# Kernel tuning notes

Hardware: AMD Instinct MI355X
Metric: run time of the kernel (lower is better)

The kernel has to match this reference:

```python
import jax, jax.numpy as jnp
import numpy as np

B, C, N = 16, 256, 2048
CK = int(C * 0.25)  # key/query channels = 64
CV = C              # value_size = 1 -> value channels = C
BN_EPS = 1e-5


def setup_inputs() -> dict:
    key = jax.random.key(0)
    ks = jax.random.split(key, 7)
    sq = lambda fan_in: 1.0 / np.sqrt(fan_in)
    x = jax.random.normal(ks[0], (B, C, N), dtype=jnp.float32)
    # Conv1d(kernel_size=1, bias=False) weights stored as [out_ch, in_ch]
    Wq = jax.random.uniform(ks[1], (CK, C), jnp.float32, -sq(C), sq(C))
    Wk = jax.random.uniform(ks[2], (CK, C), jnp.float32, -sq(C), sq(C))
    Wv = jax.random.uniform(ks[3], (CV, C), jnp.float32, -sq(C), sq(C))
    Wl = jax.random.uniform(ks[4], (C, C), jnp.float32, -sq(C), sq(C))
    gamma = jnp.ones((C,), jnp.float32)
    beta = jnp.zeros((C,), jnp.float32)
    return {"x": x, "Wq": Wq, "Wk": Wk, "Wv": Wv, "Wl": Wl,
            "gamma": gamma, "beta": beta}


def reference(x, Wq, Wk, Wv, Wl, gamma, beta):
    # x: [B, C, N]
    q = jnp.einsum('oc,bcn->bno', Wq, x)   # [B, N, CK]  (q_conv then permute)
    k = jnp.einsum('oc,bcn->bon', Wk, x)   # [B, CK, N]
    v = jnp.einsum('oc,bcn->bno', Wv, x)   # [B, N, CV]  (v_conv then permute)

    w = jnp.einsum('bnk,bkm->bnm', q, k)   # [B, N, N] raw logits
    # NOTE: column-sum divisor uses RAW logits (RHS evaluated before reassignment
    # in the torch source), not the softmax output.
    col_sum = w.sum(axis=1, keepdims=True)                 # [B, 1, N]
    s = jax.nn.softmax(w, axis=-1) / (1e-9 + col_sum)      # [B, N, N]

    att = jnp.einsum('bnm,bmc->bcn', s, v)  # [B, C, N] (matmul + permute back)
    r = x - att                              # offset (residual of attention)

    # lbr: 1x1 conv -> BatchNorm1d (training-mode batch stats) -> ReLU
    h = jnp.einsum('oc,bcn->bon', Wl, r)     # [B, C, N]
    mean = h.mean(axis=(0, 2), keepdims=True)
    var = ((h - mean) ** 2).mean(axis=(0, 2), keepdims=True)  # biased, as BN
    hn = (h - mean) * jax.lax.rsqrt(var + BN_EPS)
    bn = hn * gamma[None, :, None] + beta[None, :, None]
    out = x + jax.nn.relu(bn)
    return out
```

## Files before the change

### kernel.cpp

```cpp
#include <hip/hip_runtime.h>

#define B_ 16
#define C_ 256
#define N_ 2048
#define CK_ 64

using f32x4  = __attribute__((ext_vector_type(4))) float;
using bf16x8 = __attribute__((ext_vector_type(8))) short;
using short4_t = __attribute__((ext_vector_type(4))) short;
using u32x2  = __attribute__((ext_vector_type(2))) unsigned;

static __device__ __forceinline__ float bf2f(short s){
  unsigned u = ((unsigned)(unsigned short)s) << 16;
  float f; __builtin_memcpy(&f, &u, 4); return f;
}
static __device__ __forceinline__ short f2bf(float f){
  unsigned u; __builtin_memcpy(&u, &f, 4);
  unsigned r = (u + 0x7fffu + ((u >> 16) & 1u)) >> 16;
  return (short)(unsigned short)r;
}

static __device__ __forceinline__ int vf_off(int cp, int ck){
  int q = cp >> 1; int ch = (((cp & 1) << 2) | ck) ^ (q & 7);
  return q*128 + ch*16;
}

__global__ void k_prep(const float* __restrict__ Wq, const float* __restrict__ Wk,
                       const float* __restrict__ Wv, const float* __restrict__ Wl,
                       short* __restrict__ Wb, short* __restrict__ Wlf,
                       const float* __restrict__ x, double* __restrict__ xsum){
  int bid = blockIdx.x;
  if(bid < 1024){
    int b = bid >> 6;
    int c = (bid & 63)*4 + (threadIdx.x>>6);
    int l = threadIdx.x & 63;
    const float* row = x + ((size_t)b*C_ + c)*N_;
    double s = 0.0;
    #pragma unroll
    for(int it = 0; it < 8; ++it){
      f32x4 v = *(const f32x4*)(row + it*256 + l*4);
      s += (double)v[0] + (double)v[1] + (double)v[2] + (double)v[3];
    }
    for(int off = 32; off; off >>= 1) s += __shfl_down(s, off);
    if(l == 0) xsum[b*C_ + c] = s;
  } else {
    int i = (bid - 1024)*256 + threadIdx.x;
    if(i < 384*C_){
      int o = i >> 8;
      float v;
      if(o < 64)       v = Wq[i];
      else if(o < 128) v = Wk[i - 64*C_];
      else             v = Wv[i - 128*C_];
      Wb[i] = f2bf(v);
    }
    if(i < C_*C_){
      int o = i >> 8, c = i & 255;
      int dest = (c>>5)*8192 + (o>>4)*512 + ((((c>>3)&3)*16) + (o&15))*8 + (c&7);
      Wlf[dest] = f2bf(Wl[i]);
    }
  }
}

__global__ void k_prep_g2(const double* __restrict__ xsum, const float* __restrict__ Wq,
                          const float* __restrict__ Wk, double* __restrict__ g){
  int b = blockIdx.x;
  __shared__ double xs[C_];
  __shared__ double t[CK_];
  int tid = threadIdx.x;
  xs[tid] = xsum[b*C_ + tid];
  __syncthreads();
  if(tid < CK_){
    double s = 0.0;
    const float* wr = Wq + (size_t)tid*C_;
    for(int c = 0; c < C_; ++c) s += (double)wr[c]*xs[c];
    t[tid] = s;
  }
  __syncthreads();
  double s = 0.0;
  for(int j = 0; j < CK_; ++j) s += (double)Wk[(size_t)j*C_ + tid]*t[j];
  g[b*C_ + tid] = s;
}

#define XROW 328
__global__ __launch_bounds__(256,2) void k_qkv(const float* __restrict__ x,
        const short* __restrict__ Wb, const double* __restrict__ gg,
        short* __restrict__ qbuf, short* __restrict__ kf, short* __restrict__ vf,
        short* __restrict__ xTb){
  int b = blockIdx.y; int n0 = blockIdx.x*64;
  int tid = threadIdx.x, w = tid>>6, l = tid&63, lo = l&15, g = l>>4;
  __shared__ __attribute__((aligned(16))) short xT[64*XROW];
  __shared__ double gs[C_];
  __shared__ double csum2[256][4];
  __shared__ float inv_lds[64];
  const float* xb = x + (size_t)b*C_*N_;
  gs[tid] = gg[b*C_ + tid];
  __syncthreads();
  int pp2 = tid >> 4, cg = tid & 15;
  double cs[4] = {0.0, 0.0, 0.0, 0.0};
  #pragma unroll
  for(int cc = 0; cc < 8; ++cc){
    int ci = cc*32 + 2*pp2;
    f32x4 x0 = *(const f32x4*)(xb + (size_t)ci*N_ + n0 + 4*cg);
    f32x4 x1 = *(const f32x4*)(xb + (size_t)(ci+1)*N_ + n0 + 4*cg);
    #pragma unroll
    for(int jq = 0; jq < 4; ++jq){
      cs[jq] += (double)x0[jq]*gs[ci] + (double)x1[jq]*gs[ci+1];
      unsigned pr = (unsigned)(unsigned short)f2bf(x0[jq])
                  | (((unsigned)(unsigned short)f2bf(x1[jq]))<<16);
      *(unsigned*)(&xT[(4*cg + jq)*XROW + cc*40 + 2*pp2]) = pr;
    }
  }
  csum2[tid][0] = cs[0]; csum2[tid][1] = cs[1];
  csum2[tid][2] = cs[2]; csum2[tid][3] = cs[3];
  __syncthreads();
  if(tid < 64){
    int cgq = tid >> 2, jq = tid & 3;
    double tot = 0.0;
    #pragma unroll
    for(int k = 0; k < 16; ++k) tot += csum2[k*16 + cgq][jq];
    inv_lds[tid] = (float)(1.0/(1e-9 + tot));
  }

  f32x4 acc[6][4];
  #pragma unroll
  for(int oi=0;oi<6;++oi) for(int nj=0;nj<4;++nj) acc[oi][nj]=(f32x4){0.f,0.f,0.f,0.f};
  int n2 = tid>>2, ii2 = tid&3;
  short* xtb = xTb + ((size_t)b*N_ + n0)*C_;
  #pragma unroll
  for(int cc = 0; cc < 8; ++cc){
    *(bf16x8*)(xtb + (size_t)n2*C_ + cc*32 + 8*ii2) =
        *(const bf16x8*)(&xT[n2*XROW + cc*40 + 8*ii2]);
    bf16x8 bfr[4];
    #pragma unroll
    for(int nj = 0; nj < 4; ++nj)
      bfr[nj] = *(const bf16x8*)(&xT[(nj*16 + lo)*XROW + cc*40 + 8*g]);
    #pragma unroll
    for(int oi = 0; oi < 6; ++oi){
      int o = w*96 + oi*16 + lo;
      bf16x8 af = *(const bf16x8*)(Wb + (size_t)o*C_ + cc*32 + 8*g);
      #pragma unroll
      for(int nj = 0; nj < 4; ++nj)
        acc[oi][nj] = __builtin_amdgcn_mfma_f32_16x16x32_bf16(af, bfr[nj], acc[oi][nj], 0,0,0);
    }
  }
  __syncthreads();

  short* qb  = qbuf + (size_t)b*N_*64;
  short* kfb = kf   + (size_t)b*N_*64;
  short* vfb = vf   + (size_t)b*C_*N_;
  #pragma unroll
  for(int oi = 0; oi < 6; ++oi){
    int obase = w*96 + oi*16;
    for(int nj = 0; nj < 4; ++nj){
      int n = n0 + nj*16 + lo;
      if(obase < 64){
        short4_t pk;
        #pragma unroll
        for(int r = 0; r < 4; ++r) pk[r] = f2bf(acc[oi][nj][r]);
        *(short4_t*)(qb + (size_t)n*64 + obase + 4*g) = pk;
      } else if(obase < 128){
        int C0 = obase - 64 + 4*g;
        int mt = (n0>>4) + nj;
        int h  = C0 >> 5;
        int lanep = ((C0>>3)&3)*16 + lo;
        short4_t pk;
        #pragma unroll
        for(int r = 0; r < 4; ++r) pk[r] = f2bf(acc[oi][nj][r]);
        *(short4_t*)(kfb + ((size_t)(mt*2 + h)*64 + lanep)*8 + (C0&4)) = pk;
      } else {
        float iv = inv_lds[nj*16 + lo];
        int ckk = (n>>3)&3, wi = n&7, mc = n>>5;
        #pragma unroll
        for(int r = 0; r < 4; ++r){
          int cp = obase - 128 + 4*g + r;
          vfb[(size_t)mc*8192 + (vf_off(cp, ckk)>>1) + wi] = f2bf(acc[oi][nj][r]*iv);
        }
      }
    }
  }
}
#undef XROW

__global__ __launch_bounds__(256,2) void k_attn(const short* __restrict__ qbuf,
        const short* __restrict__ kf, const short* __restrict__ vf,
        short* __restrict__ att){
  int d = blockIdx.x;
  int xcd = d & 7, j = d >> 3;
  int b = xcd*2 + (j >> 5);
  int n0 = (j & 31)*64;
  int tid = threadIdx.x;
  int w = tid>>6, l = tid&63, lo = l&15, g = l>>4;

  __shared__ short vlds[2][16384];
  __shared__ short plds[4096];
  __shared__ float rs_lds[64];

  const short* qb  = qbuf + (size_t)b*N_*64;
  const short* kfb = kf   + (size_t)b*N_*64;
  const short* vfb = vf   + (size_t)b*C_*N_;

  bf16x8 qa0, qa1;
  {
    const short* qrow = qb + (size_t)(n0 + w*16 + lo)*64;
    qa0 = *(const bf16x8*)(qrow + 8*g);
    qa1 = *(const bf16x8*)(qrow + 32 + 8*g);
  }
  int paoff[4][2], bvoff[4][2], pw[4];
  #pragma unroll
  for(int rt = 0; rt < 4; ++rt)
    #pragma unroll
    for(int mh = 0; mh < 2; ++mh)
      paoff[rt][mh] = (rt*16 + lo)*128 + (((mh*4 + g) ^ (lo&7))*16);
  #pragma unroll
  for(int jj = 0; jj < 4; ++jj)
    #pragma unroll
    for(int mh = 0; mh < 2; ++mh)
      bvoff[jj][mh] = mh*16384 + vf_off(w*64 + jj*16 + lo, g);
  #pragma unroll
  for(int tt = 0; tt < 4; ++tt)
    pw[tt] = (w*16 + lo)*128 + (((tt*2 + (g>>1)) ^ (lo&7))*16) + (g&1)*8;

  const short* kl   = kfb + l*8;
  const short* vsrc = vfb + w*2048 + l*8;

  f32x4 oacc[4][4];
  #pragma unroll
  for(int rt=0;rt<4;++rt) for(int jj=0;jj<4;++jj) oacc[rt][jj]=(f32x4){0.f,0.f,0.f,0.f};
  float srow = 0.f;

  bf16x8 kA0,kA1,kA2,kA3,kA4,kA5,kA6,kA7;
  bf16x8 kB0,kB1,kB2,kB3,kB4,kB5,kB6,kB7;

#define LOADK(S, MC) { const short* kp = kl + (size_t)((MC)&31)*4096; \
    k##S##0 = *(const bf16x8*)(kp);        k##S##1 = *(const bf16x8*)(kp + 512); \
    k##S##2 = *(const bf16x8*)(kp + 1024); k##S##3 = *(const bf16x8*)(kp + 1536); \
    k##S##4 = *(const bf16x8*)(kp + 2048); k##S##5 = *(const bf16x8*)(kp + 2560); \
    k##S##6 = *(const bf16x8*)(kp + 3072); k##S##7 = *(const bf16x8*)(kp + 3584); }
#define GLLDS(SRC, DST) __builtin_amdgcn_global_load_lds( \
    (const __attribute__((address_space(1))) void*)(SRC), \
    (__attribute__((address_space(3))) void*)(DST), 16, 0, 0)
#define VDMA(MC, NB) { const short* vs = vsrc + (size_t)(2*(MC))*8192; \
    char* dst = (char*)&vlds[NB][0] + w*4096; \
    GLLDS(vs,        dst);        GLLDS(vs +  512, dst + 1024); \
    GLLDS(vs + 1024, dst + 2048); GLLDS(vs + 1536, dst + 3072); \
    GLLDS(vs + 8192,  dst + 16384); GLLDS(vs + 8704,  dst + 17408); \
    GLLDS(vs + 9216,  dst + 18432); GLLDS(vs + 9728,  dst + 19456); }
#define QKT(S, TT, KE, KO) { \
    f32x4 a = (f32x4){0.f,0.f,0.f,0.f}; \
    a = __builtin_amdgcn_mfma_f32_16x16x32_bf16(k##S##KE, qa0, a, 0,0,0); \
    a = __builtin_amdgcn_mfma_f32_16x16x32_bf16(k##S##KO, qa1, a, 0,0,0); \
    float e[4]; \
    _Pragma("unroll") \
    for(int r = 0; r < 4; ++r) e[r] = __builtin_exp2f(fmaf(a[r], 1.44269504f, -17.3123405f)); \
    srow += e[0]+e[1]+e[2]+e[3]; \
    unsigned p0, p1; \
    asm("v_cvt_pk_bf16_f32 %0, %1, %2" : "=v"(p0) : "v"(e[0]), "v"(e[1])); \
    asm("v_cvt_pk_bf16_f32 %0, %1, %2" : "=v"(p1) : "v"(e[2]), "v"(e[3])); \
    { u32x2 pv = {p0, p1}; *(u32x2*)((char*)&plds[0] + pw[TT]) = pv; } }

  LOADK(A, 0);
  LOADK(B, 1);
  VDMA(0, 0);

#define BODY(BUF, S, MC) { \
    VDMA(((MC)+1)&31, (BUF)^1); \
    QKT(S, 0, 0, 1); QKT(S, 1, 2, 3); QKT(S, 2, 4, 5); QKT(S, 3, 6, 7); \
    LOADK(S, (MC)+2); \
    __builtin_amdgcn_sched_barrier(0); \
    asm volatile("s_waitcnt vmcnt(16) lgkmcnt(0)" ::: "memory"); \
    __builtin_amdgcn_s_barrier(); \
    __builtin_amdgcn_sched_barrier(0); \
    __builtin_amdgcn_s_setprio(1); \
    _Pragma("unroll") \
    for(int mh = 0; mh < 2; ++mh){ \
      bf16x8 pa[4], bv[4]; \
      _Pragma("unroll") \
      for(int rt = 0; rt < 4; ++rt) pa[rt] = *(const bf16x8*)((char*)&plds[0] + paoff[rt][mh]); \
      _Pragma("unroll") \
      for(int jj = 0; jj < 4; ++jj) bv[jj] = *(const bf16x8*)((char*)&vlds[BUF][0] + bvoff[jj][mh]); \
      _Pragma("unroll") \
      for(int rt = 0; rt < 4; ++rt) \
        _Pragma("unroll") \
        for(int jj = 0; jj < 4; ++jj) \
          oacc[rt][jj] = __builtin_amdgcn_mfma_f32_16x16x32_bf16(pa[rt], bv[jj], oacc[rt][jj], 0,0,0); \
    } \
    __builtin_amdgcn_s_setprio(0); \
    __builtin_amdgcn_sched_barrier(0); \
    asm volatile("s_waitcnt lgkmcnt(0)" ::: "memory"); \
    __builtin_amdgcn_s_barrier(); \
    __builtin_amdgcn_sched_barrier(0); }

  #pragma unroll 1
  for(int it = 0; it < 16; ++it){
    BODY(0, A, 2*it);
    BODY(1, B, 2*it + 1);
  }
#undef BODY
#undef QKT
#undef VDMA
#undef GLLDS
#undef LOADK

  float S = srow;
  S += __shfl_xor(S, 16);
  S += __shfl_xor(S, 32);
  if(l < 16) rs_lds[w*16 + l] = 1.f/(S + 1e-30f);
  __syncthreads();
  float rinvs[4][4];
  #pragma unroll
  for(int rt = 0; rt < 4; ++rt)
    #pragma unroll
    for(int r = 0; r < 4; ++r) rinvs[rt][r] = rs_lds[rt*16 + 4*g + r];

  short* attb = att + (size_t)b*N_*C_;
  #pragma unroll
  for(int rt = 0; rt < 4; ++rt)
    #pragma unroll
    for(int jj = 0; jj < 4; ++jj)
      #pragma unroll
      for(int r = 0; r < 4; ++r){
        int n = n0 + rt*16 + 4*g + r;
        int c = w*64 + jj*16 + lo;
        attb[(size_t)n*C_ + c] = f2bf(oacc[rt][jj][r]*rinvs[rt][r]);
      }
}

__global__ __launch_bounds__(256,2) void k_hgemm(const short* __restrict__ xTb,
        const short* __restrict__ att, const short* __restrict__ Wlf,
        short* __restrict__ h, float* __restrict__ part){
  int b = blockIdx.y; int n0 = blockIdx.x*64;
  int bid = b*32 + blockIdx.x;
  int tid = threadIdx.x, w = tid>>6, l = tid&63, lo = l&15, g = l>>4;
  __shared__ __attribute__((aligned(16))) short rT[64*C_];
  const short* xtb = xTb + ((size_t)b*N_ + n0)*C_;
  const short* atb = att + ((size_t)b*N_ + n0)*C_;
  int half = l >> 5, ch = l & 31;
  #pragma unroll
  for(int k = 0; k < 8; ++k){
    int n = k*8 + w*2 + half;
    size_t off = (size_t)n*C_ + ch*8;
    bf16x8 xv = *(const bf16x8*)(xtb + off);
    bf16x8 av = *(const bf16x8*)(atb + off);
    bf16x8 rv;
    #pragma unroll
    for(int jq = 0; jq < 8; ++jq) rv[jq] = f2bf(bf2f(xv[jq]) - bf2f(av[jq]));
    *(bf16x8*)(&rT[n*C_ + ((ch ^ (n&7))*8)]) = rv;
  }
  __syncthreads();

  f32x4 acc[4][4];
  #pragma unroll
  for(int ot=0;ot<4;++ot) for(int nj=0;nj<4;++nj) acc[ot][nj]=(f32x4){0.f,0.f,0.f,0.f};
  #pragma unroll
  for(int cb = 0; cb < 8; ++cb){
    bf16x8 bfr[4];
    #pragma unroll
    for(int nj = 0; nj < 4; ++nj)
      bfr[nj] = *(const bf16x8*)(&rT[(nj*16 + lo)*C_ + (((cb*4 + g) ^ (lo&7))*8)]);
    #pragma unroll
    for(int ot = 0; ot < 4; ++ot){
      bf16x8 af = *(const bf16x8*)(Wlf + ((size_t)(cb*16 + w*4 + ot))*512 + l*8);
      #pragma unroll
      for(int nj = 0; nj < 4; ++nj)
        acc[ot][nj] = __builtin_amdgcn_mfma_f32_16x16x32_bf16(af, bfr[nj], acc[ot][nj], 0,0,0);
    }
  }
  short* hb = h + (size_t)b*N_*C_;
  #pragma unroll
  for(int ot = 0; ot < 4; ++ot)
    for(int nj = 0; nj < 4; ++nj){
      int n = n0 + nj*16 + lo;
      short4_t pk;
      #pragma unroll
      for(int r = 0; r < 4; ++r) pk[r] = f2bf(acc[ot][nj][r]);
      *(short4_t*)(&hb[(size_t)n*C_ + w*64 + ot*16 + 4*g]) = pk;
    }
  float* pr_ = part + (size_t)bid*512;
  #pragma unroll
  for(int ot = 0; ot < 4; ++ot){
    float s4[4] = {0,0,0,0}, q4[4] = {0,0,0,0};
    for(int nj = 0; nj < 4; ++nj)
      #pragma unroll
      for(int r = 0; r < 4; ++r){ float v = acc[ot][nj][r]; s4[r] += v; q4[r] += v*v; }
    #pragma unroll
    for(int r = 0; r < 4; ++r){
      float ss = s4[r], qq = q4[r];
      for(int msk = 1; msk < 16; msk <<= 1){ ss += __shfl_xor(ss, msk); qq += __shfl_xor(qq, msk); }
      if(lo == 0){
        int o = w*64 + ot*16 + 4*g + r;
        pr_[o] = ss;
        pr_[256 + o] = qq;
      }
    }
  }
}

__global__ void k_bnfin(const float* __restrict__ part,
                        const float* __restrict__ gamma, const float* __restrict__ beta,
                        float* __restrict__ bnsc, float* __restrict__ bnsh){
  __shared__ float ls[4][512];
  int t = threadIdx.x; int o = t & 255, seg = t >> 8;
  float s = 0.f, q = 0.f;
  for(int r = seg*128; r < seg*128 + 128; ++r){
    s += part[(size_t)r*512 + o];
    q += part[(size_t)r*512 + 256 + o];
  }
  ls[seg][o] = s; ls[seg][256 + o] = q;
  __syncthreads();
  if(t < 256){
    float S = ls[0][t] + ls[1][t] + ls[2][t] + ls[3][t];
    float Q = ls[0][256+t] + ls[1][256+t] + ls[2][256+t] + ls[3][256+t];
    float cnt = (float)(B_*N_);
    float mean = S/cnt;
    float var  = Q/cnt - mean*mean;
    float is   = rsqrtf(var + 1e-5f);
    float sc   = gamma[t]*is;
    bnsc[t] = sc;
    bnsh[t] = beta[t] - mean*sc;
  }
}

__global__ void k_final(const float* __restrict__ x, const short* __restrict__ h,
                        const float* __restrict__ bnsc, const float* __restrict__ bnsh,
                        float* __restrict__ out){
  int b = blockIdx.z, c0 = blockIdx.y*64, n0 = blockIdx.x*64;
  int tid = threadIdx.x;
  __shared__ float ht[64][65];
  {
    int n = tid>>2, ii = tid&3;
    #pragma unroll
    for(int p = 0; p < 2; ++p){
      int coff = 32*p + 8*ii;
      bf16x8 hv = *(const bf16x8*)(h + ((size_t)(b*N_ + n0 + n))*C_ + c0 + coff);
      #pragma unroll
      for(int jq = 0; jq < 8; ++jq) ht[n][coff + jq] = bf2f(hv[jq]);
    }
  }
  __syncthreads();
  int c = tid>>2, i2 = tid&3;
  float sc = bnsc[c0 + c], sh = bnsh[c0 + c];
  const float* xr = x + ((size_t)b*C_ + c0 + c)*N_ + n0 + 16*i2;
  float* orow = out + ((size_t)b*C_ + c0 + c)*N_ + n0 + 16*i2;
  #pragma unroll
  for(int k = 0; k < 16; k += 4){
    f32x4 xv = *(const f32x4*)(xr + k);
    f32x4 ov;
    #pragma unroll
    for(int jq = 0; jq < 4; ++jq){
      float bn = ht[16*i2 + k + jq][c]*sc + sh;
      ov[jq] = xv[jq] + fmaxf(bn, 0.f);
    }
    *(f32x4*)(orow + k) = ov;
  }
}

extern "C" void kernel_launch(void* const* d_in, const int* in_sizes, int n_in,
                              void* d_out, int out_size, void* d_ws, size_t ws_size,
                              hipStream_t stream){
  const float* x     = (const float*)d_in[0];
  const float* Wq    = (const float*)d_in[1];
  const float* Wk    = (const float*)d_in[2];
  const float* Wv    = (const float*)d_in[3];
  const float* Wl    = (const float*)d_in[4];
  const float* gamma = (const float*)d_in[5];
  const float* beta  = (const float*)d_in[6];
  float* out = (float*)d_out;

  char* p = (char*)d_ws;
  double* g    = (double*)p; p += (size_t)B_*C_*8;
  double* xsum = (double*)p; p += (size_t)B_*C_*8;
  short* Wb   = (short*)p;  p += (size_t)384*C_*2;
  short* Wlf  = (short*)p;  p += (size_t)C_*C_*2;
  short* qbuf = (short*)p;  p += (size_t)B_*N_*64*2;
  short* kf   = (short*)p;  p += (size_t)B_*N_*64*2;
  short* vf   = (short*)p;  p += (size_t)B_*C_*N_*2;
  short* xTb  = (short*)p;  p += (size_t)B_*N_*C_*2;
  short* att  = (short*)p;  p += (size_t)B_*N_*C_*2;
  float* part = (float*)p;  p += (size_t)512*512*4;
  float* bnsc = (float*)p;  p += C_*4;
  float* bnsh = (float*)p;  p += C_*4;
  short* h = vf;

  k_prep   <<<1408, 256, 0, stream>>>(Wq, Wk, Wv, Wl, Wb, Wlf, x, xsum);
  k_prep_g2<<<B_, 256, 0, stream>>>(xsum, Wq, Wk, g);
  k_qkv    <<<dim3(N_/64, B_), 256, 0, stream>>>(x, Wb, g, qbuf, kf, vf, xTb);
  k_attn   <<<512, 256, 0, stream>>>(qbuf, kf, vf, att);
  k_hgemm  <<<dim3(N_/64, B_), 256, 0, stream>>>(xTb, att, Wlf, h, part);
  k_bnfin  <<<1, 1024, 0, stream>>>(part, gamma, beta, bnsc, bnsh);
  k_final  <<<dim3(N_/64, C_/64, B_), 256, 0, stream>>>(x, h, bnsc, bnsh, out);
}
```

Baseline: 143.8 us.

## Store h channel-major from hgemm via LDS transpose, simplify final kernel

The hgemm kernel now writes h in [B,C,N] layout, transposing accumulators through the reused LDS tile with a swizzle and storing 16-byte coalesced rows. The final BN/ReLU/residual kernel then becomes a simple row-wise streaming kernel with no LDS transpose or sync. This moves the transpose cost into hgemm, adding two barriers and LDS traffic there, in exchange for cheaper, fully coalesced epilogue loads and stores.

```diff
diff --git a/kernel.cpp b/kernel.cpp
--- a/kernel.cpp
+++ b/kernel.cpp
@@ -327,7 +327,7 @@
 
 __global__ __launch_bounds__(256,2) void k_hgemm(const short* __restrict__ xTb,
         const short* __restrict__ att, const short* __restrict__ Wlf,
-        short* __restrict__ h, float* __restrict__ part){
+        short* __restrict__ hT, float* __restrict__ part){
   int b = blockIdx.y; int n0 = blockIdx.x*64;
   int bid = b*32 + blockIdx.x;
   int tid = threadIdx.x, w = tid>>6, l = tid&63, lo = l&15, g = l>>4;
@@ -365,16 +365,6 @@
         acc[ot][nj] = __builtin_amdgcn_mfma_f32_16x16x32_bf16(af, bfr[nj], acc[ot][nj], 0,0,0);
     }
   }
-  short* hb = h + (size_t)b*N_*C_;
-  #pragma unroll
-  for(int ot = 0; ot < 4; ++ot)
-    for(int nj = 0; nj < 4; ++nj){
-      int n = n0 + nj*16 + lo;
-      short4_t pk;
-      #pragma unroll
-      for(int r = 0; r < 4; ++r) pk[r] = f2bf(acc[ot][nj][r]);
-      *(short4_t*)(&hb[(size_t)n*C_ + w*64 + ot*16 + 4*g]) = pk;
-    }
   float* pr_ = part + (size_t)bid*512;
   #pragma unroll
   for(int ot = 0; ot < 4; ++ot){
@@ -391,6 +381,28 @@
         pr_[o] = ss;
         pr_[256 + o] = qq;
       }
+    }
+  }
+  __syncthreads();
+  #pragma unroll
+  for(int ot = 0; ot < 4; ++ot)
+    #pragma unroll
+    for(int nj = 0; nj < 4; ++nj)
+      #pragma unroll
+      for(int r = 0; r < 4; ++r){
+        int o = w*64 + ot*16 + 4*g + r;
+        int n = nj*16 + lo;
+        rT[o*64 + (n ^ (((o>>2)&3)*16))] = f2bf(acc[ot][nj][r]);
+      }
+  __syncthreads();
+  short* hTb = hT + (size_t)b*C_*N_ + n0;
+  {
+    int ro = tid >> 3, li = tid & 7;
+    #pragma unroll
+    for(int pss = 0; pss < 8; ++pss){
+      int o = pss*32 + ro;
+      bf16x8 v = *(const bf16x8*)(&rT[o*64 + ((li*8) ^ (((o>>2)&3)*16))]);
+      *(bf16x8*)(hTb + (size_t)o*N_ + li*8) = v;
     }
   }
 }
@@ -420,38 +432,27 @@
   }
 }
 
-__global__ void k_final(const float* __restrict__ x, const short* __restrict__ h,
+__global__ void k_final(const float* __restrict__ x, const short* __restrict__ hT,
                         const float* __restrict__ bnsc, const float* __restrict__ bnsh,
                         float* __restrict__ out){
-  int b = blockIdx.z, c0 = blockIdx.y*64, n0 = blockIdx.x*64;
-  int tid = threadIdx.x;
-  __shared__ float ht[64][65];
-  {
-    int n = tid>>2, ii = tid&3;
-    #pragma unroll
-    for(int p = 0; p < 2; ++p){
-      int coff = 32*p + 8*ii;
-      bf16x8 hv = *(const bf16x8*)(h + ((size_t)(b*N_ + n0 + n))*C_ + c0 + coff);
-      #pragma unroll
-      for(int jq = 0; jq < 8; ++jq) ht[n][coff + jq] = bf2f(hv[jq]);
-    }
-  }
-  __syncthreads();
-  int c = tid>>2, i2 = tid&3;
-  float sc = bnsc[c0 + c], sh = bnsh[c0 + c];
-  const float* xr = x + ((size_t)b*C_ + c0 + c)*N_ + n0 + 16*i2;
-  float* orow = out + ((size_t)b*C_ + c0 + c)*N_ + n0 + 16*i2;
-  #pragma unroll
-  for(int k = 0; k < 16; k += 4){
-    f32x4 xv = *(const f32x4*)(xr + k);
-    f32x4 ov;
-    #pragma unroll
-    for(int jq = 0; jq < 4; ++jq){
-      float bn = ht[16*i2 + k + jq][c]*sc + sh;
-      ov[jq] = xv[jq] + fmaxf(bn, 0.f);
-    }
-    *(f32x4*)(orow + k) = ov;
-  }
+  int row = blockIdx.x;
+  int c = row & 255;
+  float sc = bnsc[c], sh = bnsh[c];
+  const short* hr = hT + (size_t)row*N_;
+  const float* xr = x + (size_t)row*N_;
+  float* orow = out + (size_t)row*N_;
+  int t = threadIdx.x;
+  bf16x8 hv = *(const bf16x8*)(hr + t*8);
+  f32x4 x0 = *(const f32x4*)(xr + t*8);
+  f32x4 x1 = *(const f32x4*)(xr + t*8 + 4);
+  f32x4 o0, o1;
+  #pragma unroll
+  for(int jq = 0; jq < 4; ++jq){
+    o0[jq] = x0[jq] + fmaxf(fmaf(bf2f(hv[jq]), sc, sh), 0.f);
+    o1[jq] = x1[jq] + fmaxf(fmaf(bf2f(hv[jq+4]), sc, sh), 0.f);
+  }
+  *(f32x4*)(orow + t*8) = o0;
+  *(f32x4*)(orow + t*8 + 4) = o1;
 }
 
 extern "C" void kernel_launch(void* const* d_in, const int* in_sizes, int n_in,
@@ -479,13 +480,13 @@
   float* part = (float*)p;  p += (size_t)512*512*4;
   float* bnsc = (float*)p;  p += C_*4;
   float* bnsh = (float*)p;  p += C_*4;
-  short* h = vf;
+  short* hT = vf;
 
   k_prep   <<<1408, 256, 0, stream>>>(Wq, Wk, Wv, Wl, Wb, Wlf, x, xsum);
   k_prep_g2<<<B_, 256, 0, stream>>>(xsum, Wq, Wk, g);
   k_qkv    <<<dim3(N_/64, B_), 256, 0, stream>>>(x, Wb, g, qbuf, kf, vf, xTb);
   k_attn   <<<512, 256, 0, stream>>>(qbuf, kf, vf, att);
-  k_hgemm  <<<dim3(N_/64, B_), 256, 0, stream>>>(xTb, att, Wlf, h, part);
+  k_hgemm  <<<dim3(N_/64, B_), 256, 0, stream>>>(xTb, att, Wlf, hT, part);
   k_bnfin  <<<1, 1024, 0, stream>>>(part, gamma, beta, bnsc, bnsh);
-  k_final  <<<dim3(N_/64, C_/64, B_), 256, 0, stream>>>(x, h, bnsc, bnsh, out);
-}
+  k_final  <<<4096, 256, 0, stream>>>(x, hT, bnsc, bnsh, out);
+}
```

New measurement: 138.2 us. -3.9%, faster.
